# Optimization experiments

Measured on AMD Instinct MI355X. Metric: run time of the kernel, lower is better.

## Reference

```python
import jax, jax.numpy as jnp
import numpy as np

BATCH, NODE_NUM, SEQ_LEN, FEATURE_NUM = 256, 256, 128, 64
HIDDEN, FC_HIDDEN = 1024, 512
BN_EPS = 1e-5
LEAKY_SLOPE = 0.01


def setup_inputs() -> dict:
    key = jax.random.key(0)
    ks = jax.random.split(key, 16)
    # feature part of x: [B, S, feature_num-1]
    feats = jax.random.normal(ks[0], (BATCH, SEQ_LEN, FEATURE_NUM - 1), dtype=jnp.float32)
    # unique station ids per sample (torch loop overwrites on duplicates; unique ids make scatter well-defined)
    sid = jax.vmap(lambda k: jax.random.permutation(k, NODE_NUM)[:SEQ_LEN])(jax.random.split(ks[1], BATCH))
    extra = jax.random.normal(ks[2], (BATCH, SEQ_LEN, 1), dtype=jnp.float32)
    # x layout: [features (F-1) | station_id | extra] -> last dim = FEATURE_NUM + 1, id at index -2
    x = jnp.concatenate([feats, sid[..., None].astype(jnp.float32), extra], axis=-1)
    # random symmetric binary adjacency
    adj = (jax.random.uniform(ks[3], (NODE_NUM, NODE_NUM)) < 0.05).astype(jnp.float32)
    adj_mat = jnp.maximum(adj, adj.T)
    s = 0.02
    return {
        "x": x,
        "adj_mat": adj_mat,
        "W1": jax.random.normal(ks[4], (FEATURE_NUM - 1, HIDDEN // 2)) * s,
        "b1": jnp.zeros((HIDDEN // 2,), jnp.float32),
        "W2": jax.random.normal(ks[5], (HIDDEN // 2, HIDDEN // 2)) * s,
        "b2": jnp.zeros((HIDDEN // 2,), jnp.float32),
        "W3": jax.random.normal(ks[6], (HIDDEN // 2, HIDDEN)) * s,
        "b3": jnp.zeros((HIDDEN,), jnp.float32),
        "fcW1": jax.random.normal(ks[7], (HIDDEN, FC_HIDDEN)) * s,
        "fcb1": jnp.zeros((FC_HIDDEN,), jnp.float32),
        "gamma": jnp.ones((FC_HIDDEN,), jnp.float32),
        "beta": jnp.zeros((FC_HIDDEN,), jnp.float32),
        "fcW2": jax.random.normal(ks[8], (FC_HIDDEN, 1)) * s,
        "fcb2": jnp.zeros((1,), jnp.float32),
    }


def _normalize_adj(adj_mat):
    A = adj_mat + jnp.eye(NODE_NUM, dtype=adj_mat.dtype)
    d_inv_sqrt = 1.0 / jnp.sqrt(jnp.sum(A, axis=1))  # D^{-1/2}
    return d_inv_sqrt[:, None] * A * d_inv_sqrt[None, :]


def reference(x, adj_mat, W1, b1, W2, b2, W3, b3, fcW1, fcb1, gamma, beta, fcW2, fcb2):
    An = _normalize_adj(adj_mat)  # [N, N]
    sid = x[:, :, -2].astype(jnp.int32)            # [B, S]
    g_sid = x[:, -1, -2].astype(jnp.int32)         # [B]
    b_idx = jnp.arange(BATCH)
    # scatter node features by station id: X[i, sid[i,j]] = x[i, j, :-2]
    X = jnp.zeros((BATCH, NODE_NUM, FEATURE_NUM - 1), x.dtype)
    X = X.at[b_idx[:, None], sid].set(x[:, :, :-2])
    # three rounds of A @ X -> Linear -> ReLU
    X = jax.nn.relu(jnp.einsum("nm,bmf->bnf", An, X) @ W1 + b1)
    X = jax.nn.relu(jnp.einsum("nm,bmf->bnf", An, X) @ W2 + b2)
    X = jax.nn.relu(jnp.einsum("nm,bmf->bnf", An, X) @ W3 + b3)  # [B, N, HIDDEN]
    # gather per-sample station feature
    g = X[b_idx, g_sid]                            # [B, HIDDEN]
    # FC head: Linear -> BatchNorm1d (training stats) -> LeakyReLU -> Linear -> Sigmoid
    h = g @ fcW1 + fcb1
    mean = jnp.mean(h, axis=0)
    var = jnp.var(h, axis=0)  # biased, as used by torch BN for normalization
    h = (h - mean) * jax.lax.rsqrt(var + BN_EPS) * gamma + beta
    h = jnp.where(h >= 0, h, LEAKY_SLOPE * h)
    return jax.nn.sigmoid(h @ fcW2 + fcb2)         # [B, 1]
```

## Files before the change

### kernel.cpp

```cpp
#include <hip/hip_runtime.h>
#include <cstdint>
#include <initializer_list>

#define B_   256
#define N_   256
#define S_   128
#define Fm1  63
#define XROW 65
#define H1   512
#define H2   1024
#define FCH  512
#define NCAP 64

typedef __attribute__((ext_vector_type(8))) short short8;
typedef __attribute__((ext_vector_type(4))) float f32x4;

__device__ __forceinline__ unsigned short f2bf(float f) {
    union { float f; unsigned u; } v; v.f = f;
    unsigned r = v.u + 0x7FFF + ((v.u >> 16) & 1);
    return (unsigned short)(r >> 16);
}
__device__ __forceinline__ float bf2f(unsigned short u) {
    union { unsigned u; float f; } v; v.u = ((unsigned)u) << 16;
    return v.f;
}

__global__ void k_dinv(const float* __restrict__ adj, float* __restrict__ dinv) {
    int n = blockIdx.x;
    float s = 0.f;
    for (int m = threadIdx.x; m < N_; m += 64) s += adj[n * N_ + m];
    for (int off = 32; off; off >>= 1) s += __shfl_down(s, off);
    if (threadIdx.x == 0) dinv[n] = rsqrtf(s + 1.0f);
}

__global__ void k_an(const float* __restrict__ adj, const float* __restrict__ dinv,
                     unsigned short* __restrict__ Anb) {
    int i = blockIdx.x * 256 + threadIdx.x;
    int n = i >> 8, m = i & 255;
    float a = adj[i] + (n == m ? 1.f : 0.f);
    Anb[i] = f2bf(a * dinv[n] * dinv[m]);
}

__global__ void k_nbr(const float* __restrict__ adj, const float* __restrict__ dinv,
                      const float* __restrict__ x,
                      int* __restrict__ nidx, float* __restrict__ nw) {
    int b = blockIdx.x;
    int lane = threadIdx.x;
    int g = (int)x[((size_t)b * S_ + S_ - 1) * XROW + (XROW - 2)];
    float dg = dinv[g];
    int base = 0;
    for (int c = 0; c < 4; ++c) {
        int m = c * 64 + lane;
        float a = adj[g * N_ + m] + (g == m ? 1.f : 0.f);
        float v = a * dg * dinv[m];
        unsigned long long mask = __ballot(v != 0.f);
        int pos = __popcll(mask & ((1ull << lane) - 1ull));
        if (v != 0.f) {
            int s = base + pos;
            if (s < NCAP) { nidx[b * NCAP + s] = m; nw[b * NCAP + s] = v; }
        }
        base += __popcll(mask);
    }
    for (int s = base + lane; s < NCAP; s += 64) {
        nidx[b * NCAP + s] = 0;
        nw[b * NCAP + s] = 0.f;
    }
}

__global__ void k_cvtT4(const float* __restrict__ W1, const float* __restrict__ W2,
                        const float* __restrict__ W3, const float* __restrict__ fcW1,
                        unsigned short* __restrict__ W1T, unsigned short* __restrict__ W2T,
                        unsigned short* __restrict__ W3T, unsigned short* __restrict__ fcW1T) {
    const float* in; unsigned short* out; int R_in, C_in, R_pad;
    switch (blockIdx.z) {
        case 0:  in = W1;   out = W1T;   R_in = Fm1; C_in = H1; R_pad = 64;  break;
        case 1:  in = W2;   out = W2T;   R_in = H1;  C_in = H1; R_pad = H1;  break;
        case 2:  in = W3;   out = W3T;   R_in = H1;  C_in = H2; R_pad = H1;  break;
        default: in = fcW1; out = fcW1T; R_in = H2;  C_in = H1; R_pad = H2;  break;
    }
    int r0 = blockIdx.y * 32, c0 = blockIdx.x * 32;
    if (r0 >= R_pad || c0 >= C_in) return;
    __shared__ float tile[32][33];
    int tr = threadIdx.x >> 5, tc = threadIdx.x & 31;
#pragma unroll
    for (int rr = 0; rr < 4; ++rr) {
        int r = r0 + tr + rr * 8;
        tile[tr + rr * 8][tc] = (r < R_in) ? in[(size_t)r * C_in + c0 + tc] : 0.f;
    }
    __syncthreads();
#pragma unroll
    for (int rr = 0; rr < 4; ++rr) {
        int c = c0 + tr + rr * 8;
        int r = r0 + tc;
        out[(size_t)c * R_pad + r] = f2bf(tile[tc][tr + rr * 8]);
    }
}

__global__ void k_zero(uint4* __restrict__ p, int n16) {
    int i = blockIdx.x * 256 + threadIdx.x;
    if (i < n16) p[i] = uint4{0, 0, 0, 0};
}

__global__ void k_scatter(const float* __restrict__ x, unsigned short* __restrict__ Xs) {
    int idx = blockIdx.x * 256 + threadIdx.x;
    int f8 = idx & 7;
    int j  = (idx >> 3) & 127;
    int b  = idx >> 10;
    const float* row = x + ((size_t)b * S_ + j) * XROW;
    int s = (int)row[XROW - 2];
    const float* src = row + f8 * 8;
    unsigned short o[8];
#pragma unroll
    for (int i = 0; i < 8; ++i) {
        int f = f8 * 8 + i;
        o[i] = (f < Fm1) ? f2bf(src[i]) : (unsigned short)0;
    }
    *(uint4*)(Xs + ((size_t)s * B_ + b) * 64 + f8 * 8) = *(uint4*)o;
}

template <int ACT, int BIAS>
__global__ __launch_bounds__(256) void bgemm(const unsigned short* __restrict__ A,
                                             const unsigned short* __restrict__ B,
                                             const float* __restrict__ bias,
                                             unsigned short* __restrict__ C,
                                             int K, int lda, int ldb, int ldc) {
    __shared__ unsigned short Abuf[2][4][128][8];
    __shared__ unsigned short Bbuf[2][4][128][8];
    int tid = threadIdx.x;
    int bm = blockIdx.y * 128, bn = blockIdx.x * 128;
    int wid = tid >> 6, lane = tid & 63;
    int wr = wid >> 1, wc = wid & 1;
    int arow = tid >> 1, ahalf = tid & 1;
    int bcol = (tid & 63) * 2, bkb = tid >> 6;
    f32x4 acc[4][4] = {};
    uint4 areg0, areg1;
    unsigned br0[4], br1[4];
    const int nt = K / 32;
    auto gload = [&](int t) {
        int k0 = t * 32;
        const unsigned short* ap = A + (size_t)(bm + arow) * lda + k0 + ahalf * 16;
        areg0 = *(const uint4*)(ap);
        areg1 = *(const uint4*)(ap + 8);
        const unsigned short* bp = B + (size_t)(k0 + bkb * 8) * ldb + bn + bcol;
#pragma unroll
        for (int jj = 0; jj < 4; ++jj) {
            unsigned lo = *(const unsigned*)(bp);
            unsigned hi = *(const unsigned*)(bp + ldb);
            br0[jj] = (lo & 0xffffu) | (hi << 16);
            br1[jj] = (lo >> 16) | (hi & 0xffff0000u);
            bp += 2 * (size_t)ldb;
        }
    };
    auto swrite = [&](int buf) {
        *(uint4*)(&Abuf[buf][ahalf * 2 + 0][arow][0]) = areg0;
        *(uint4*)(&Abuf[buf][ahalf * 2 + 1][arow][0]) = areg1;
        *(uint4*)(&Bbuf[buf][bkb][bcol][0]) = *(uint4*)br0;
        *(uint4*)(&Bbuf[buf][bkb][bcol + 1][0]) = *(uint4*)br1;
    };
    gload(0);
    swrite(0);
    __syncthreads();
    for (int t = 0; t < nt; ++t) {
        if (t + 1 < nt) gload(t + 1);
        int buf = t & 1;
        int kb = lane >> 4, lr = lane & 15;
        short8 af[4], bfr[4];
#pragma unroll
        for (int i = 0; i < 4; ++i)
            af[i] = *(const short8*)(&Abuf[buf][kb][wr * 64 + i * 16 + lr][0]);
#pragma unroll
        for (int j = 0; j < 4; ++j)
            bfr[j] = *(const short8*)(&Bbuf[buf][kb][wc * 64 + j * 16 + lr][0]);
#pragma unroll
        for (int i = 0; i < 4; ++i)
#pragma unroll
            for (int j = 0; j < 4; ++j)
                acc[i][j] = __builtin_amdgcn_mfma_f32_16x16x32_bf16(
                    af[i], bfr[j], acc[i][j], 0, 0, 0);
        if (t + 1 < nt) swrite(buf ^ 1);
        __syncthreads();
    }
    int lr = lane & 15, rg = lane >> 4;
#pragma unroll
    for (int j = 0; j < 4; ++j) {
        int col = bn + wc * 64 + j * 16 + lr;
        float bv = BIAS ? bias[col] : 0.f;
#pragma unroll
        for (int i = 0; i < 4; ++i) {
            int row0 = bm + wr * 64 + i * 16 + rg * 4;
#pragma unroll
            for (int r = 0; r < 4; ++r) {
                float v = acc[i][j][r] + bv;
                if (ACT) v = fmaxf(v, 0.f);
                C[(size_t)(row0 + r) * ldc + col] = f2bf(v);
            }
        }
    }
}

template <int ACT, int BIASMODE, int OUTF32>
__global__ __launch_bounds__(256) void btgemm(const unsigned short* __restrict__ A,
                                              const unsigned short* __restrict__ Bm,
                                              const float* __restrict__ bias,
                                              void* __restrict__ Cv,
                                              int K, int lda, int ldb, int ldc,
                                              int ns, int sb, int sc) {
    __shared__ unsigned short Ab[2][128][32];
    __shared__ unsigned short Bb[2][128][32];
    int tid = threadIdx.x;
    int bm = blockIdx.y * 128;
    int bx = blockIdx.x;
    int sample = bx >> ns;
    int bn = (bx & ((1 << ns) - 1)) * 128;
    const unsigned short* Bp = Bm + (size_t)sample * sb;
    size_t coff = (size_t)sample * sc;

    int wid = tid >> 6, lane = tid & 63;
    int wr = wid >> 1, wc = wid & 1;
    int c0 = wid * 2;
    int lrow = lane >> 2, lkq = lane & 3;

    f32x4 acc[4][4] = {};
    const int nt = K / 32;

    auto STAGE = [&](int t, int buf) {
        int k0 = t * 32;
#pragma unroll
        for (int i = 0; i < 2; ++i) {
            int row = (c0 + i) * 16 + lrow;
            const unsigned short* ga = A + (size_t)(bm + row) * lda + k0 + lkq * 8;
            __builtin_amdgcn_global_load_lds(
                (const __attribute__((address_space(1))) unsigned int*)ga,
                (__attribute__((address_space(3))) unsigned int*)&Ab[buf][(c0 + i) * 16][0],
                16, 0, 0);
            const unsigned short* gb = Bp + (size_t)(bn + row) * ldb + k0 + lkq * 8;
            __builtin_amdgcn_global_load_lds(
                (const __attribute__((address_space(1))) unsigned int*)gb,
                (__attribute__((address_space(3))) unsigned int*)&Bb[buf][(c0 + i) * 16][0],
                16, 0, 0);
        }
    };

    STAGE(0, 0);
    __syncthreads();
    int kb = lane >> 4, lr = lane & 15;
    for (int t = 0; t < nt; ++t) {
        int buf = t & 1;
        if (t + 1 < nt) STAGE(t + 1, buf ^ 1);
        short8 af[4], bfr[4];
#pragma unroll
        for (int i = 0; i < 4; ++i)
            af[i] = *(const short8*)&Ab[buf][wr * 64 + i * 16 + lr][kb * 8];
#pragma unroll
        for (int j = 0; j < 4; ++j)
            bfr[j] = *(const short8*)&Bb[buf][wc * 64 + j * 16 + lr][kb * 8];
#pragma unroll
        for (int i = 0; i < 4; ++i)
#pragma unroll
            for (int j = 0; j < 4; ++j)
                acc[i][j] = __builtin_amdgcn_mfma_f32_16x16x32_bf16(
                    af[i], bfr[j], acc[i][j], 0, 0, 0);
        __syncthreads();
    }
    int rg = lane >> 4;
#pragma unroll
    for (int j = 0; j < 4; ++j) {
        int col = bn + wc * 64 + j * 16 + lr;
        float bcv = (BIASMODE == 1) ? bias[col] : 0.f;
#pragma unroll
        for (int i = 0; i < 4; ++i) {
            int row0 = bm + wr * 64 + i * 16 + rg * 4;
#pragma unroll
            for (int r = 0; r < 4; ++r) {
                float v = acc[i][j][r];
                if (BIASMODE == 1) v += bcv;
                if (BIASMODE == 2) v += bias[row0 + r];
                if (ACT) v = fmaxf(v, 0.f);
                if (OUTF32)
                    ((float*)Cv)[coff + (size_t)(row0 + r) * ldc + col] = v;
                else
                    ((unsigned short*)Cv)[coff + (size_t)(row0 + r) * ldc + col] = f2bf(v);
            }
        }
    }
}

__global__ __launch_bounds__(256) void k_l1t1(
    const unsigned short* __restrict__ Anb,
    const int* __restrict__ nidx,
    const unsigned short* __restrict__ T0,
    const unsigned short* __restrict__ W1T,
    const float* __restrict__ b1,
    unsigned short* __restrict__ T1r) {
    int bi = blockIdx.x;
    int b = (bi & 7) + 8 * (bi >> 5);
    int hq = (bi >> 3) & 3;
    int tid = threadIdx.x, w = tid >> 6, lane = tid & 63;
    int lr = lane & 15, kb = lane >> 4, rg = lane >> 4;
    __shared__ unsigned short Asub[NCAP * 256];
    __shared__ unsigned short T0s[2][64 * 64];
    __shared__ unsigned short X1s[128 * 64];
    for (int c = tid; c < NCAP * 32; c += 256) {
        int s = c >> 5, q = c & 31;
        int m = nidx[b * NCAP + s];
        uint4 v = *(const uint4*)(Anb + (size_t)m * 256 + q * 8);
        *(uint4*)((char*)Asub + s * 512 + ((q * 16) ^ ((s & 7) << 4))) = v;
    }
    short8 wfr[8][2];
    float b1v[8];
#pragma unroll
    for (int hj = 0; hj < 8; ++hj) {
        int h = hq * 128 + hj * 16 + lr;
        b1v[hj] = b1[h];
#pragma unroll
        for (int ks = 0; ks < 2; ++ks)
            wfr[hj][ks] = *(const short8*)(W1T + (size_t)h * 64 + ks * 32 + kb * 8);
    }
    auto STAGE = [&](int q, int buf) {
#pragma unroll
        for (int j = 0; j < 2; ++j) {
            int slot = j * 4 + w;
            int mloc = slot * 8 + (lane >> 3);
            int qg = (lane & 7) ^ (lane >> 3);
            const unsigned short* src =
                T0 + (size_t)(q * 64 + mloc) * (B_ * 64) + b * 64 + qg * 8;
            __builtin_amdgcn_global_load_lds(
                (const __attribute__((address_space(1))) unsigned int*)src,
                (__attribute__((address_space(3))) unsigned int*)(&T0s[buf][slot * 512]),
                16, 0, 0);
        }
    };
    STAGE(0, 0);
    __syncthreads();
    f32x4 acc2[4][2] = {};
    int buf = 0;
    for (int q = 0; q < 4; ++q) {
        if (q < 3) STAGE(q + 1, buf ^ 1);
        f32x4 acc[8] = {};
        const char* t0b = (const char*)&T0s[buf][0];
#pragma unroll
        for (int ks = 0; ks < 2; ++ks) {
            short8 af = *(const short8*)(t0b + (w * 16 + lr) * 128 +
                                         ((ks * 64 + kb * 16) ^ ((lr & 7) << 4)));
#pragma unroll
            for (int hj = 0; hj < 8; ++hj)
                acc[hj] = __builtin_amdgcn_mfma_f32_16x16x32_bf16(
                    af, wfr[hj][ks], acc[hj], 0, 0, 0);
        }
        asm volatile("s_waitcnt vmcnt(0)" ::: "memory");
        __syncthreads();
#pragma unroll
        for (int hj = 0; hj < 8; ++hj) {
            int h = hj * 16 + lr;
            unsigned short pk[4];
#pragma unroll
            for (int r = 0; r < 4; ++r)
                pk[r] = f2bf(fmaxf(acc[hj][r] + b1v[hj], 0.f));
            int m0 = w * 16 + rg * 4;
            *(uint2*)((char*)X1s + h * 128 + ((m0 * 2) ^ ((h & 7) << 4))) = *(uint2*)pk;
        }
        __syncthreads();
#pragma unroll
        for (int ks2 = 0; ks2 < 2; ++ks2) {
            short8 af2[4];
#pragma unroll
            for (int ai = 0; ai < 4; ++ai)
                af2[ai] = *(const short8*)((char*)Asub + (ai * 16 + lr) * 512 +
                                           ((q * 128 + ks2 * 64 + kb * 16) ^ ((lr & 7) << 4)));
#pragma unroll
            for (int hj2 = 0; hj2 < 2; ++hj2) {
                int h = w * 32 + hj2 * 16 + lr;
                short8 bf2 = *(const short8*)((char*)X1s + h * 128 +
                                              ((ks2 * 64 + kb * 16) ^ ((h & 7) << 4)));
#pragma unroll
                for (int ai = 0; ai < 4; ++ai)
                    acc2[ai][hj2] = __builtin_amdgcn_mfma_f32_16x16x32_bf16(
                        af2[ai], bf2, acc2[ai][hj2], 0, 0, 0);
            }
        }
        __syncthreads();
        buf ^= 1;
    }
#pragma unroll
    for (int hj2 = 0; hj2 < 2; ++hj2) {
        int h = hq * 128 + w * 32 + hj2 * 16 + lr;
#pragma unroll
        for (int ai = 0; ai < 4; ++ai) {
#pragma unroll
            for (int r = 0; r < 4; ++r) {
                int i = ai * 16 + rg * 4 + r;
                T1r[(size_t)(b * NCAP + i) * H1 + h] = f2bf(acc2[ai][hj2][r]);
            }
        }
    }
}

__global__ __launch_bounds__(256) void k_x2y(
    const unsigned short* __restrict__ T1r,
    const unsigned short* __restrict__ W2T,
    const float* __restrict__ b2,
    const float* __restrict__ nw,
    unsigned short* __restrict__ y) {
    __shared__ unsigned short Ab[2][128][32];
    __shared__ unsigned short Bb[2][128][32];
    int tid = threadIdx.x;
    int i0 = blockIdx.x;
    int bm = ((i0 & 7) + 8 * (i0 >> 5)) * 128;
    int bn = ((i0 >> 3) & 3) * 128;
    int wid = tid >> 6, lane = tid & 63;
    int wr = wid >> 1, wc = wid & 1;
    int c0 = wid * 2;
    int lrow = lane >> 2, lkq = lane & 3;
    f32x4 acc[4][4] = {};
    const int nt = H1 / 32;
    auto STAGE = [&](int t, int buf) {
        int k0 = t * 32;
#pragma unroll
        for (int i = 0; i < 2; ++i) {
            int row = (c0 + i) * 16 + lrow;
            const unsigned short* ga = T1r + (size_t)(bm + row) * H1 + k0 + lkq * 8;
            __builtin_amdgcn_global_load_lds(
                (const __attribute__((address_space(1))) unsigned int*)ga,
                (__attribute__((address_space(3))) unsigned int*)&Ab[buf][(c0 + i) * 16][0],
                16, 0, 0);
            const unsigned short* gb = W2T + (size_t)(bn + row) * H1 + k0 + lkq * 8;
            __builtin_amdgcn_global_load_lds(
                (const __attribute__((address_space(1))) unsigned int*)gb,
                (__attribute__((address_space(3))) unsigned int*)&Bb[buf][(c0 + i) * 16][0],
                16, 0, 0);
        }
    };
    STAGE(0, 0);
    __syncthreads();
    int kb = lane >> 4, lr = lane & 15;
    for (int t = 0; t < nt; ++t) {
        int buf = t & 1;
        if (t + 1 < nt) STAGE(t + 1, buf ^ 1);
        short8 af[4], bfr[4];
#pragma unroll
        for (int i = 0; i < 4; ++i)
            af[i] = *(const short8*)&Ab[buf][wr * 64 + i * 16 + lr][kb * 8];
#pragma unroll
        for (int j = 0; j < 4; ++j)
            bfr[j] = *(const short8*)&Bb[buf][wc * 64 + j * 16 + lr][kb * 8];
#pragma unroll
        for (int i = 0; i < 4; ++i)
#pragma unroll
            for (int j = 0; j < 4; ++j)
                acc[i][j] = __builtin_amdgcn_mfma_f32_16x16x32_bf16(
                    af[i], bfr[j], acc[i][j], 0, 0, 0);
        __syncthreads();
    }
    int rg = lane >> 4;
    int s = (bm >> 6) + wr;
    float wv[4][4];
#pragma unroll
    for (int i = 0; i < 4; ++i)
#pragma unroll
        for (int r = 0; r < 4; ++r)
            wv[i][r] = nw[s * NCAP + i * 16 + rg * 4 + r];
#pragma unroll
    for (int j = 0; j < 4; ++j) {
        int col = bn + wc * 64 + j * 16 + lr;
        float bcv = b2[col];
        float p = 0.f;
#pragma unroll
        for (int i = 0; i < 4; ++i)
#pragma unroll
            for (int r = 0; r < 4; ++r)
                p += wv[i][r] * fmaxf(acc[i][j][r] + bcv, 0.f);
        p += __shfl_xor(p, 16);
        p += __shfl_xor(p, 32);
        if (rg == 0) y[(size_t)s * H1 + col] = f2bf(p);
    }
}

__global__ void k_bnstats(const float* __restrict__ h, float* __restrict__ mv) {
    int c = blockIdx.x * 64 + (threadIdx.x & 63);
    int grp = threadIdx.x >> 6;
    float s = 0.f, s2 = 0.f;
    for (int b = grp * 64; b < grp * 64 + 64; ++b) {
        float v = h[(size_t)b * FCH + c];
        s += v; s2 += v * v;
    }
    __shared__ float rs[4][64], rq[4][64];
    rs[grp][c & 63] = s;
    rq[grp][c & 63] = s2;
    __syncthreads();
    if (grp == 0) {
        float S = rs[0][c & 63] + rs[1][c & 63] + rs[2][c & 63] + rs[3][c & 63];
        float Q = rq[0][c & 63] + rq[1][c & 63] + rq[2][c & 63] + rq[3][c & 63];
        float mean = S * (1.f / B_);
        float var = Q * (1.f / B_) - mean * mean;
        mv[c] = mean;
        mv[FCH + c] = rsqrtf(var + 1e-5f);
    }
}

__global__ void k_head(const float* __restrict__ h, const float* __restrict__ mv,
                       const float* __restrict__ gamma, const float* __restrict__ beta,
                       const float* __restrict__ fcW2, const float* __restrict__ fcb2,
                       float* __restrict__ out) {
    int b = blockIdx.x, t = threadIdx.x;
    float v = h[(size_t)b * FCH + t];
    v = (v - mv[t]) * mv[FCH + t] * gamma[t] + beta[t];
    v = (v >= 0.f) ? v : 0.01f * v;
    float p = v * fcW2[t];
    __shared__ float red[8];
    for (int off = 32; off; off >>= 1) p += __shfl_down(p, off);
    if ((t & 63) == 0) red[t >> 6] = p;
    __syncthreads();
    if (t == 0) {
        float s = fcb2[0];
#pragma unroll
        for (int i = 0; i < 8; ++i) s += red[i];
        out[b] = 1.f / (1.f + expf(-s));
    }
}

static inline size_t align256(size_t x) { return (x + 255) & ~(size_t)255; }

extern "C" void kernel_launch(void* const* d_in, const int* in_sizes, int n_in,
                              void* d_out, int out_size, void* d_ws, size_t ws_size,
                              hipStream_t stream) {
    const float* x     = (const float*)d_in[0];
    const float* adj   = (const float*)d_in[1];
    const float* W1    = (const float*)d_in[2];
    const float* b1    = (const float*)d_in[3];
    const float* W2    = (const float*)d_in[4];
    const float* b2    = (const float*)d_in[5];
    const float* W3    = (const float*)d_in[6];
    const float* b3    = (const float*)d_in[7];
    const float* fcW1  = (const float*)d_in[8];
    const float* fcb1  = (const float*)d_in[9];
    const float* gamma = (const float*)d_in[10];
    const float* beta  = (const float*)d_in[11];
    const float* fcW2  = (const float*)d_in[12];
    const float* fcb2  = (const float*)d_in[13];
    float* out = (float*)d_out;

    char* ws = (char*)d_ws;
    size_t off = 0;
    auto alloc = [&](size_t bytes) { char* p = ws + off; off += align256(bytes); return p; };
    unsigned short* Anb   = (unsigned short*)alloc((size_t)N_ * N_ * 2);
    float*          dinv  = (float*)alloc((size_t)N_ * 4);
    int*            nidx  = (int*)alloc((size_t)B_ * NCAP * 4);
    float*          nw    = (float*)alloc((size_t)B_ * NCAP * 4);
    unsigned short* W1T   = (unsigned short*)alloc((size_t)H1 * 64 * 2);
    unsigned short* W2T   = (unsigned short*)alloc((size_t)H1 * H1 * 2);
    unsigned short* W3T   = (unsigned short*)alloc((size_t)H2 * H1 * 2);
    unsigned short* fcW1T = (unsigned short*)alloc((size_t)H1 * H2 * 2);
    unsigned short* y     = (unsigned short*)alloc((size_t)B_ * H1 * 2);
    unsigned short* g     = (unsigned short*)alloc((size_t)B_ * H2 * 2);
    float*          h     = (float*)alloc((size_t)B_ * FCH * 4);
    float*          mv    = (float*)alloc((size_t)1024 * 4);
    unsigned short* Xs    = (unsigned short*)alloc((size_t)N_ * B_ * 64 * 2);
    unsigned short* T0    = (unsigned short*)alloc((size_t)N_ * B_ * 64 * 2);
    unsigned short* T1r   = (unsigned short*)alloc((size_t)B_ * NCAP * H1 * 2);
    if (off > ws_size) return;

    k_dinv<<<N_, 64, 0, stream>>>(adj, dinv);
    k_an<<<N_, 256, 0, stream>>>(adj, dinv, Anb);
    k_nbr<<<B_, 64, 0, stream>>>(adj, dinv, x, nidx, nw);
    k_cvtT4<<<dim3(32, 32, 4), 256, 0, stream>>>(W1, W2, W3, fcW1, W1T, W2T, W3T, fcW1T);

    {
        int n16 = (N_ * B_ * 64) / 8;
        k_zero<<<(n16 + 255) / 256, 256, 0, stream>>>((uint4*)Xs, n16);
        k_scatter<<<(B_ * S_ * 8) / 256, 256, 0, stream>>>(x, Xs);
    }

    bgemm<0, 0><<<dim3((B_ * 64) / 128, 2), 256, 0, stream>>>(
        Anb, Xs, nullptr, T0, N_, N_, B_ * 64, B_ * 64);

    k_l1t1<<<B_ * 4, 256, 0, stream>>>(Anb, nidx, T0, W1T, b1, T1r);

    k_x2y<<<(B_ * NCAP / 128) * (H1 / 128), 256, 0, stream>>>(
        T1r, W2T, b2, nw, y);

    btgemm<1, 1, 0><<<dim3(H2 / 128, B_ / 128), 256, 0, stream>>>(
        y, W3T, b3, g, H1, H1, H1, H2, 20, 0, 0);

    btgemm<0, 1, 1><<<dim3(FCH / 128, B_ / 128), 256, 0, stream>>>(
        g, fcW1T, fcb1, h, H2, H2, H2, FCH, 20, 0, 0);

    k_bnstats<<<FCH / 64, 256, 0, stream>>>(h, mv);
    k_head<<<B_, FCH, 0, stream>>>(h, mv, gamma, beta, fcW2, fcb2, out);
}
```

Before: 128.6 us.

## Fuse prep kernels, merge zero+scatter, fold BN stats into GEMM epilogue

Cuts the launch count in three places. The adjacency normalization and neighbor extraction now run in one kernel with dinv cached in shared memory. Zeroing and scattering are merged into a per-sample kernel that writes every Xs row exactly once. BatchNorm sums and sums of squares are accumulated with atomics in the last GEMM's epilogue, and the head kernel finishes the mean and variance, so the separate stats kernel and the full zero pass over Xs are removed. The trade-offs are atomic contention, a different float summation order, and a sum-of-squares variance that is less precise.

```diff
diff --git a/kernel.cpp b/kernel.cpp
--- a/kernel.cpp
+++ b/kernel.cpp
@@ -25,45 +25,54 @@
     return v.f;
 }
 
-__global__ void k_dinv(const float* __restrict__ adj, float* __restrict__ dinv) {
+__global__ void k_dinv(const float* __restrict__ adj, float* __restrict__ dinv,
+                       float* __restrict__ mv) {
     int n = blockIdx.x;
+    if (n == N_) {
+        for (int k = threadIdx.x; k < 1024; k += 64) mv[k] = 0.f;
+        return;
+    }
     float s = 0.f;
     for (int m = threadIdx.x; m < N_; m += 64) s += adj[n * N_ + m];
     for (int off = 32; off; off >>= 1) s += __shfl_down(s, off);
     if (threadIdx.x == 0) dinv[n] = rsqrtf(s + 1.0f);
 }
 
-__global__ void k_an(const float* __restrict__ adj, const float* __restrict__ dinv,
-                     unsigned short* __restrict__ Anb) {
-    int i = blockIdx.x * 256 + threadIdx.x;
-    int n = i >> 8, m = i & 255;
-    float a = adj[i] + (n == m ? 1.f : 0.f);
-    Anb[i] = f2bf(a * dinv[n] * dinv[m]);
-}
-
-__global__ void k_nbr(const float* __restrict__ adj, const float* __restrict__ dinv,
-                      const float* __restrict__ x,
-                      int* __restrict__ nidx, float* __restrict__ nw) {
-    int b = blockIdx.x;
-    int lane = threadIdx.x;
-    int g = (int)x[((size_t)b * S_ + S_ - 1) * XROW + (XROW - 2)];
-    float dg = dinv[g];
-    int base = 0;
-    for (int c = 0; c < 4; ++c) {
-        int m = c * 64 + lane;
-        float a = adj[g * N_ + m] + (g == m ? 1.f : 0.f);
-        float v = a * dg * dinv[m];
-        unsigned long long mask = __ballot(v != 0.f);
-        int pos = __popcll(mask & ((1ull << lane) - 1ull));
-        if (v != 0.f) {
-            int s = base + pos;
-            if (s < NCAP) { nidx[b * NCAP + s] = m; nw[b * NCAP + s] = v; }
-        }
-        base += __popcll(mask);
-    }
-    for (int s = base + lane; s < NCAP; s += 64) {
-        nidx[b * NCAP + s] = 0;
-        nw[b * NCAP + s] = 0.f;
+__global__ void k_prep(const float* __restrict__ adj, const float* __restrict__ dinv,
+                       const float* __restrict__ x,
+                       unsigned short* __restrict__ Anb,
+                       int* __restrict__ nidx, float* __restrict__ nw) {
+    __shared__ float dl[N_];
+    int tid = threadIdx.x;
+    dl[tid] = dinv[tid];
+    __syncthreads();
+    int blk = blockIdx.x;
+    if (blk < N_) {
+        int n = blk;
+        float a = adj[n * N_ + tid] + (n == tid ? 1.f : 0.f);
+        Anb[n * N_ + tid] = f2bf(a * dl[n] * dl[tid]);
+    } else {
+        int w = tid >> 6, lane = tid & 63;
+        int b = (blk - N_) * 4 + w;
+        int g = (int)x[((size_t)b * S_ + S_ - 1) * XROW + (XROW - 2)];
+        float dg = dl[g];
+        int base = 0;
+        for (int c = 0; c < 4; ++c) {
+            int m = c * 64 + lane;
+            float a = adj[g * N_ + m] + (g == m ? 1.f : 0.f);
+            float v = a * dg * dl[m];
+            unsigned long long mask = __ballot(v != 0.f);
+            int pos = __popcll(mask & ((1ull << lane) - 1ull));
+            if (v != 0.f) {
+                int s = base + pos;
+                if (s < NCAP) { nidx[b * NCAP + s] = m; nw[b * NCAP + s] = v; }
+            }
+            base += __popcll(mask);
+        }
+        for (int s = base + lane; s < NCAP; s += 64) {
+            nidx[b * NCAP + s] = 0;
+            nw[b * NCAP + s] = 0.f;
+        }
     }
 }
 
@@ -96,26 +105,35 @@
     }
 }
 
-__global__ void k_zero(uint4* __restrict__ p, int n16) {
-    int i = blockIdx.x * 256 + threadIdx.x;
-    if (i < n16) p[i] = uint4{0, 0, 0, 0};
-}
-
-__global__ void k_scatter(const float* __restrict__ x, unsigned short* __restrict__ Xs) {
-    int idx = blockIdx.x * 256 + threadIdx.x;
-    int f8 = idx & 7;
-    int j  = (idx >> 3) & 127;
-    int b  = idx >> 10;
-    const float* row = x + ((size_t)b * S_ + j) * XROW;
-    int s = (int)row[XROW - 2];
-    const float* src = row + f8 * 8;
-    unsigned short o[8];
-#pragma unroll
-    for (int i = 0; i < 8; ++i) {
-        int f = f8 * 8 + i;
-        o[i] = (f < Fm1) ? f2bf(src[i]) : (unsigned short)0;
-    }
-    *(uint4*)(Xs + ((size_t)s * B_ + b) * 64 + f8 * 8) = *(uint4*)o;
+__global__ void k_scatter0(const float* __restrict__ x, unsigned short* __restrict__ Xs) {
+    int b = blockIdx.x, tid = threadIdx.x;
+    __shared__ short pres[N_];
+    pres[tid] = -1;
+    __syncthreads();
+    if (tid < S_) {
+        int s = (int)x[((size_t)b * S_ + tid) * XROW + (XROW - 2)];
+        pres[s] = (short)tid;
+    }
+    __syncthreads();
+#pragma unroll
+    for (int pass = 0; pass < 8; ++pass) {
+        int m = pass * 32 + (tid >> 3);
+        int f8 = tid & 7;
+        int j = pres[m];
+        unsigned short o[8];
+        if (j >= 0) {
+            const float* src = x + ((size_t)b * S_ + j) * XROW + f8 * 8;
+#pragma unroll
+            for (int i = 0; i < 8; ++i) {
+                int f = f8 * 8 + i;
+                o[i] = (f < Fm1) ? f2bf(src[i]) : (unsigned short)0;
+            }
+        } else {
+#pragma unroll
+            for (int i = 0; i < 8; ++i) o[i] = 0;
+        }
+        *(uint4*)(Xs + ((size_t)m * B_ + b) * 64 + f8 * 8) = *(uint4*)o;
+    }
 }
 
 template <int ACT, int BIAS>
@@ -198,11 +216,12 @@
     }
 }
 
-template <int ACT, int BIASMODE, int OUTF32>
+template <int ACT, int BIASMODE, int OUTF32, int BNACC>
 __global__ __launch_bounds__(256) void btgemm(const unsigned short* __restrict__ A,
                                               const unsigned short* __restrict__ Bm,
                                               const float* __restrict__ bias,
                                               void* __restrict__ Cv,
+                                              float* __restrict__ bnacc,
                                               int K, int lda, int ldb, int ldc,
                                               int ns, int sb, int sc) {
     __shared__ unsigned short Ab[2][128][32];
@@ -267,6 +286,7 @@
     for (int j = 0; j < 4; ++j) {
         int col = bn + wc * 64 + j * 16 + lr;
         float bcv = (BIASMODE == 1) ? bias[col] : 0.f;
+        float ps = 0.f, pq = 0.f;
 #pragma unroll
         for (int i = 0; i < 4; ++i) {
             int row0 = bm + wr * 64 + i * 16 + rg * 4;
@@ -280,6 +300,15 @@
                     ((float*)Cv)[coff + (size_t)(row0 + r) * ldc + col] = v;
                 else
                     ((unsigned short*)Cv)[coff + (size_t)(row0 + r) * ldc + col] = f2bf(v);
+                if (BNACC) { ps += v; pq += v * v; }
+            }
+        }
+        if (BNACC) {
+            ps += __shfl_xor(ps, 16); ps += __shfl_xor(ps, 32);
+            pq += __shfl_xor(pq, 16); pq += __shfl_xor(pq, 32);
+            if (rg == 0) {
+                atomicAdd(&bnacc[col], ps);
+                atomicAdd(&bnacc[FCH + col], pq);
             }
         }
     }
@@ -475,35 +504,15 @@
     }
 }
 
-__global__ void k_bnstats(const float* __restrict__ h, float* __restrict__ mv) {
-    int c = blockIdx.x * 64 + (threadIdx.x & 63);
-    int grp = threadIdx.x >> 6;
-    float s = 0.f, s2 = 0.f;
-    for (int b = grp * 64; b < grp * 64 + 64; ++b) {
-        float v = h[(size_t)b * FCH + c];
-        s += v; s2 += v * v;
-    }
-    __shared__ float rs[4][64], rq[4][64];
-    rs[grp][c & 63] = s;
-    rq[grp][c & 63] = s2;
-    __syncthreads();
-    if (grp == 0) {
-        float S = rs[0][c & 63] + rs[1][c & 63] + rs[2][c & 63] + rs[3][c & 63];
-        float Q = rq[0][c & 63] + rq[1][c & 63] + rq[2][c & 63] + rq[3][c & 63];
-        float mean = S * (1.f / B_);
-        float var = Q * (1.f / B_) - mean * mean;
-        mv[c] = mean;
-        mv[FCH + c] = rsqrtf(var + 1e-5f);
-    }
-}
-
 __global__ void k_head(const float* __restrict__ h, const float* __restrict__ mv,
                        const float* __restrict__ gamma, const float* __restrict__ beta,
                        const float* __restrict__ fcW2, const float* __restrict__ fcb2,
                        float* __restrict__ out) {
     int b = blockIdx.x, t = threadIdx.x;
+    float mean = mv[t] * (1.f / B_);
+    float rstd = rsqrtf(mv[FCH + t] * (1.f / B_) - mean * mean + 1e-5f);
     float v = h[(size_t)b * FCH + t];
-    v = (v - mv[t]) * mv[FCH + t] * gamma[t] + beta[t];
+    v = (v - mean) * rstd * gamma[t] + beta[t];
     v = (v >= 0.f) ? v : 0.01f * v;
     float p = v * fcW2[t];
     __shared__ float red[8];
@@ -559,31 +568,18 @@
     unsigned short* T1r   = (unsigned short*)alloc((size_t)B_ * NCAP * H1 * 2);
     if (off > ws_size) return;
 
-    k_dinv<<<N_, 64, 0, stream>>>(adj, dinv);
-    k_an<<<N_, 256, 0, stream>>>(adj, dinv, Anb);
-    k_nbr<<<B_, 64, 0, stream>>>(adj, dinv, x, nidx, nw);
+    k_dinv<<<N_ + 1, 64, 0, stream>>>(adj, dinv, mv);
     k_cvtT4<<<dim3(32, 32, 4), 256, 0, stream>>>(W1, W2, W3, fcW1, W1T, W2T, W3T, fcW1T);
-
-    {
-        int n16 = (N_ * B_ * 64) / 8;
-        k_zero<<<(n16 + 255) / 256, 256, 0, stream>>>((uint4*)Xs, n16);
-        k_scatter<<<(B_ * S_ * 8) / 256, 256, 0, stream>>>(x, Xs);
-    }
-
+    k_prep<<<N_ + B_ / 4, 256, 0, stream>>>(adj, dinv, x, Anb, nidx, nw);
+    k_scatter0<<<B_, 256, 0, stream>>>(x, Xs);
     bgemm<0, 0><<<dim3((B_ * 64) / 128, 2), 256, 0, stream>>>(
         Anb, Xs, nullptr, T0, N_, N_, B_ * 64, B_ * 64);
-
     k_l1t1<<<B_ * 4, 256, 0, stream>>>(Anb, nidx, T0, W1T, b1, T1r);
-
     k_x2y<<<(B_ * NCAP / 128) * (H1 / 128), 256, 0, stream>>>(
         T1r, W2T, b2, nw, y);
-
-    btgemm<1, 1, 0><<<dim3(H2 / 128, B_ / 128), 256, 0, stream>>>(
-        y, W3T, b3, g, H1, H1, H1, H2, 20, 0, 0);
-
-    btgemm<0, 1, 1><<<dim3(FCH / 128, B_ / 128), 256, 0, stream>>>(
-        g, fcW1T, fcb1, h, H2, H2, H2, FCH, 20, 0, 0);
-
-    k_bnstats<<<FCH / 64, 256, 0, stream>>>(h, mv);
+    btgemm<1, 1, 0, 0><<<dim3(H2 / 128, B_ / 128), 256, 0, stream>>>(
+        y, W3T, b3, g, nullptr, H1, H1, H1, H2, 20, 0, 0);
+    btgemm<0, 1, 1, 1><<<dim3(FCH / 128, B_ / 128), 256, 0, stream>>>(
+        g, fcW1T, fcb1, h, mv, H2, H2, H2, FCH, 20, 0, 0);
     k_head<<<B_, FCH, 0, stream>>>(h, mv, gamma, beta, fcW2, fcb2, out);
 }
```

Result: faster. 111.7 us (-13.2%).
